# Kernel tuning notes

Hardware: AMD Instinct MI355X
Metric: run time of the kernel (lower is better)

The kernel has to match this reference:

```python
import jax, jax.numpy as jnp
import numpy as np
from jax import lax

B, N, K, NUM_CLASS = 8, 4096, 16, 13


def knn(pc, k):
    # pc: (B, C, N); returns indices of k nearest neighbors (B, N, k)
    sq = jnp.sum(pc * pc, axis=1)                       # (B, N)
    inner = jnp.einsum('bcn,bcm->bnm', pc, pc)          # (B, N, N)
    neg_dist = 2.0 * inner - sq[:, :, None] - sq[:, None, :]
    return lax.top_k(neg_dist, k)[1]                    # (B, N, k)


def group(fea, idx):
    # fea: (B, C, N), idx: (B, N, k) -> (B, C, N, k)
    return jax.vmap(lambda f, i: f[:, i])(fea, idx)


def mlp2(x, w, b, act=True):
    # 1x1 conv2d: x (B, Cin, N, k) -> (B, Cout, N, k)
    y = jnp.einsum('oc,bcnk->bonk', w, x) + b[None, :, None, None]
    return jax.nn.relu(y) if act else y


def mlp1(x, w, b, act=True):
    # 1x1 conv1d: x (B, Cin, N) -> (B, Cout, N)
    y = jnp.einsum('oc,bcn->bon', w, x) + b[None, :, None]
    return jax.nn.relu(y) if act else y


def edgeconv(xyz, fea, k, wg1, bg1, wg2, bg2, wf1, bf1, wf2, bf2, wf3, bf3):
    idx = knn(fea, k)
    # geometric branch: (B, 10, N, k) = [dist, xyz, xyz_knn, xyz - xyz_knn]
    xk = group(xyz, idx)
    xc = jnp.broadcast_to(xyz[:, :, :, None], xk.shape)
    xr = xc - xk
    xd = jnp.sqrt(jnp.sum(xr * xr, axis=1, keepdims=True))
    g = jnp.concatenate([xd, xc, xk, xr], axis=1)
    # feature branch: (B, 2C, N, k) = [fea, fea_knn]
    fk = group(fea, idx)
    fc = jnp.broadcast_to(fea[:, :, :, None], fk.shape)
    f = jnp.concatenate([fc, fk], axis=1)
    g = mlp2(mlp2(g, wg1, bg1), wg2, bg2)
    f = mlp2(mlp2(mlp2(f, wf1, bf1), wf2, bf2), wf3, bf3)
    return jnp.max(g * f, axis=-1)  # (B, Cout, N)


_SPECS = [
    ('e1_mg1', 10, 32), ('e1_mg2', 32, 32),
    ('e1_mf1', 6, 32), ('e1_mf2', 32, 32), ('e1_mf3', 32, 32),
    ('e2_mg1', 10, 128), ('e2_mg2', 128, 128),
    ('e2_mf1', 64, 128), ('e2_mf2', 128, 128), ('e2_mf3', 128, 128),
    ('c1', 128, 128), ('c2', 128, 1024), ('c3', 1184, 512),
    ('c4', 512, 256), ('c5', 256, 128), ('c6', 128, NUM_CLASS),
]


def setup_inputs() -> dict:
    key = jax.random.key(0)
    ks = jax.random.split(key, 2 * len(_SPECS) + 1)
    inp = {'xyz': jax.random.normal(ks[0], (B, N, 3), dtype=jnp.float32)}
    for j, (name, ci, co) in enumerate(_SPECS):
        scale = 1.0 / np.sqrt(ci)
        inp['w_' + name] = jax.random.normal(ks[2 * j + 1], (co, ci), dtype=jnp.float32) * scale
        inp['b_' + name] = jax.random.normal(ks[2 * j + 2], (co,), dtype=jnp.float32) * 0.01
    return inp


def reference(xyz, w_e1_mg1, b_e1_mg1, w_e1_mg2, b_e1_mg2, w_e1_mf1, b_e1_mf1,
              w_e1_mf2, b_e1_mf2, w_e1_mf3, b_e1_mf3, w_e2_mg1, b_e2_mg1,
              w_e2_mg2, b_e2_mg2, w_e2_mf1, b_e2_mf1, w_e2_mf2, b_e2_mf2,
              w_e2_mf3, b_e2_mf3, w_c1, b_c1, w_c2, b_c2, w_c3, b_c3,
              w_c4, b_c4, w_c5, b_c5, w_c6, b_c6):
    x = jnp.transpose(xyz, (0, 2, 1))  # (B, 3, N)
    fea1 = edgeconv(x, x, K, w_e1_mg1, b_e1_mg1, w_e1_mg2, b_e1_mg2,
                    w_e1_mf1, b_e1_mf1, w_e1_mf2, b_e1_mf2, w_e1_mf3, b_e1_mf3)
    fea2 = edgeconv(x, fea1, K, w_e2_mg1, b_e2_mg1, w_e2_mg2, b_e2_mg2,
                    w_e2_mf1, b_e2_mf1, w_e2_mf2, b_e2_mf2, w_e2_mf3, b_e2_mf3)
    f = mlp1(fea2, w_c1, b_c1)
    f = mlp1(f, w_c2, b_c2)                        # (B, 1024, N)
    g = jnp.max(f, axis=-1, keepdims=True)         # global feature (B, 1024, 1)
    g = jnp.broadcast_to(g, (g.shape[0], g.shape[1], x.shape[2]))
    f = jnp.concatenate([fea1, fea2, g], axis=1)   # (B, 1184, N)
    f = mlp1(f, w_c3, b_c3)
    f = mlp1(f, w_c4, b_c4)
    f = mlp1(f, w_c5, b_c5)
    return mlp1(f, w_c6, b_c6, act=False)          # (B, NUM_CLASS, N)
```

## Files before the change

kernel.cpp:

```cpp
#include <hip/hip_runtime.h>
#include <math.h>

#define B_ 8
#define N_ 4096
#define PL_ (8 * 4096 * 32)

__device__ __forceinline__ unsigned short bf16rne(float x) {
    unsigned int u = __float_as_uint(x);
    return (unsigned short)((u + 0x7FFFu + ((u >> 16) & 1u)) >> 16);
}
__device__ __forceinline__ float bff(unsigned short h) {
    return __uint_as_float((unsigned int)h << 16);
}
__device__ __forceinline__ void cvt_hl(unsigned short* base, int numel, int idx, float x) {
    unsigned short h = bf16rne(x);
    base[idx] = h;
    base[numel + idx] = bf16rne(x - bff(h));
}

typedef __attribute__((ext_vector_type(8))) short bf16x8;
typedef __attribute__((ext_vector_type(4))) float f32x4;

#define MF16(a, b, c) __builtin_amdgcn_mfma_f32_16x16x32_bf16((a), (b), (c), 0, 0, 0)

__global__ __launch_bounds__(256) void prep_kernel(
    const float* __restrict__ w0, const float* __restrict__ w1,
    const float* __restrict__ w2, const float* __restrict__ w3,
    const float* __restrict__ w4, const float* __restrict__ w5,
    const float* __restrict__ w6, const float* __restrict__ w8,
    const float* __restrict__ w9, const float* __restrict__ w10,
    const float* __restrict__ w11, const float* __restrict__ w12,
    const float* __restrict__ w13, const float* __restrict__ w14,
    const float* __restrict__ wf1, const float* __restrict__ bf1,
    const float* __restrict__ xyz,
    float* __restrict__ wt, float* __restrict__ gbuf, float* __restrict__ sqbuf,
    unsigned short* __restrict__ xyzp) {
    const int g = blockIdx.x * 256 + threadIdx.x;
    unsigned short* wus = (unsigned short*)(wt + 3840);

    if (g < 3584) {
        if (g < 320)       { int i = g >> 5, o = g & 31;             wt[g] = w0[o * 10 + i]; }
        else if (g < 1344) { int l = g - 320;  int i = l >> 5, o = l & 31; wt[g] = w1[o * 32 + i]; }
        else if (g < 1536) { int l = g - 1344; int i = l >> 5, o = l & 31; wt[g] = w2[o * 6 + i]; }
        else if (g < 2560) { int l = g - 1536; int i = l >> 5, o = l & 31; wt[g] = w3[o * 32 + i]; }
        else               { int l = g - 2560; int i = l >> 5, o = l & 31; wt[g] = w4[o * 32 + i]; }
    }
    else if (g < 3840)   { int l = g - 3584; wt[g] = (l < 128) ? bf1[l] : 0.0f; }
    else if (g < 12032)  { int l = g - 3840; int o = l >> 5, i = l & 31;
                           float x = (o < 128) ? wf1[o * 64 + i] : wf1[(o - 128) * 64 + 32 + i];
                           cvt_hl(wus + 0, 8192, l, x); }
    else if (g < 28416)  { int l = g - 12032;  cvt_hl(wus + 16384, 16384, l, w10[l]); }
    else if (g < 159488) { int l = g - 28416;  cvt_hl(wus + 49152, 131072, l, w11[l]); }
    else if (g < 241408) { int l = g - 159488; int o = l / 160, i = l - o * 160;
                           cvt_hl(wus + 311296, 81920, l, w12[o * 1184 + i]); }
    else if (g < 372480) { int l = g - 241408; cvt_hl(wus + 475136, 131072, l, w13[l]); }
    else if (g < 405248) { int l = g - 372480; cvt_hl(wus + 737280, 32768, l, w14[l]); }
    else if (g < 409344) { int l = g - 405248; int o = l >> 5, k = l & 31;
                           float x = (k < 10) ? w5[o * 10 + k] : 0.0f;
                           cvt_hl(wus + 802816, 4096, l, x); }
    else if (g < 425728) { int l = g - 409344; cvt_hl(wus + 811008, 16384, l, w6[l]); }
    else if (g < 442112) { int l = g - 425728; cvt_hl(wus + 843776, 16384, l, w8[l]); }
    else if (g < 458496) { int l = g - 442112; cvt_hl(wus + 876544, 16384, l, w9[l]); }
    else if (g < 466688) { gbuf[g - 458496] = 0.0f; }
    else if (g < 499456) { int l = g - 466688;
                           const float* p = xyz + (size_t)l * 3;
                           sqbuf[l] = fmaf(p[0], p[0], fmaf(p[1], p[1], p[2] * p[2])); }
    else if (g < 532224) {
        int row = g - 499456;
        const float* p = xyz + (size_t)row * 3;
        unsigned short hv[8] = {0,0,0,0,0,0,0,0};
        unsigned short mv[8] = {0,0,0,0,0,0,0,0};
        unsigned short lv[8] = {0,0,0,0,0,0,0,0};
        #pragma unroll
        for (int c = 0; c < 3; ++c) {
            float v = p[c];
            unsigned short h = bf16rne(v); float d = v - bff(h);
            unsigned short m = bf16rne(d);
            hv[c] = h; mv[c] = m; lv[c] = bf16rne(d - bff(m));
        }
        uint4 z = make_uint4(0u, 0u, 0u, 0u);
        unsigned short* d0 = xyzp + (size_t)row * 32;
        unsigned short* d1 = d0 + PL_;
        unsigned short* d2 = d0 + 2 * PL_;
        *(uint4*)d0 = *(uint4*)hv; *(uint4*)(d0 + 8) = z; *(uint4*)(d0 + 16) = z; *(uint4*)(d0 + 24) = z;
        *(uint4*)d1 = *(uint4*)mv; *(uint4*)(d1 + 8) = z; *(uint4*)(d1 + 16) = z; *(uint4*)(d1 + 24) = z;
        *(uint4*)d2 = *(uint4*)lv; *(uint4*)(d2 + 8) = z; *(uint4*)(d2 + 16) = z; *(uint4*)(d2 + 24) = z;
    }
}

__global__ __launch_bounds__(256) void fea1p_kernel(
    const float* __restrict__ F, unsigned short* __restrict__ P, float* __restrict__ SQ) {
    int row = blockIdx.x * 256 + threadIdx.x;
    const float* x = F + (size_t)row * 32;
    float s = 0.0f;
    unsigned short hb[32], mb[32], lb[32];
    #pragma unroll
    for (int c = 0; c < 32; ++c) {
        float v = x[c];
        s = fmaf(v, v, s);
        unsigned short h = bf16rne(v); float d = v - bff(h);
        unsigned short m = bf16rne(d);
        hb[c] = h; mb[c] = m; lb[c] = bf16rne(d - bff(m));
    }
    SQ[row] = s;
    unsigned short* d0 = P + (size_t)row * 32;
    #pragma unroll
    for (int q = 0; q < 4; ++q) {
        *(uint4*)(d0 + 8 * q)           = *(uint4*)&hb[8 * q];
        *(uint4*)(d0 + PL_ + 8 * q)     = *(uint4*)&mb[8 * q];
        *(uint4*)(d0 + 2 * PL_ + 8 * q) = *(uint4*)&lb[8 * q];
    }
}


__device__ __forceinline__ void cas_asc(unsigned long long& x, unsigned long long& y) {
    unsigned long long a = x, b = y;
    bool sw = a > b;
    x = sw ? b : a;
    y = sw ? a : b;
}

__device__ __forceinline__ void merge_top(unsigned long long (&k)[16],
                                          const unsigned long long (&o)[16]) {
    #pragma unroll
    for (int i = 0; i < 16; ++i) {
        unsigned long long bb = o[15 - i];
        if (bb > k[i]) k[i] = bb;
    }
    #pragma unroll
    for (int st = 8; st >= 1; st >>= 1)
        #pragma unroll
        for (int i = 0; i < 16; ++i)
            if ((i & st) == 0) cas_asc(k[i], k[i + st]);
}

__device__ __forceinline__ void merge_idx_row(
    const unsigned long long* __restrict__ Kbuf, int b, int row, int* __restrict__ dst) {
    unsigned long long K0[16], K1[16];
    const unsigned long long* p0 = Kbuf + (((size_t)b * 2 + 0) * N_ + row) * 16;
    const unsigned long long* p1 = Kbuf + (((size_t)b * 2 + 1) * N_ + row) * 16;
    #pragma unroll
    for (int j = 0; j < 16; ++j) { K0[j] = p0[j]; K1[j] = p1[j]; }
    merge_top(K0, K1);
    #pragma unroll
    for (int j = 0; j < 16; ++j)
        dst[j] = 4095 - (int)(unsigned int)(K0[15 - j] & 0xFFFFFFFFu);
}

__device__ __forceinline__ void casv(float& x, float& y) {
    float lo = fminf(x, y), hi = fmaxf(x, y);
    x = lo; y = hi;
}

__device__ __forceinline__ void sortv16(float (&v)[16]) {
    #pragma unroll
    for (int sz = 2; sz <= 16; sz <<= 1)
        #pragma unroll
        for (int st = sz >> 1; st >= 1; st >>= 1)
            #pragma unroll
            for (int i = 0; i < 16; ++i)
                if ((i & st) == 0) {
                    if ((i & sz) == 0) casv(v[i], v[i + st]);
                    else                casv(v[i + st], v[i]);
                }
}

__device__ __forceinline__ void mergev(float (&kv)[16], const float (&nv)[16]) {
    #pragma unroll
    for (int i = 0; i < 16; ++i) kv[i] = fmaxf(kv[i], nv[15 - i]);
    #pragma unroll
    for (int st = 8; st >= 1; st >>= 1)
        #pragma unroll
        for (int i = 0; i < 16; ++i)
            if ((i & st) == 0) casv(kv[i], kv[i + st]);
}

__global__ __launch_bounds__(512, 2) void knn_kernel(
    const unsigned short* __restrict__ P, const float* __restrict__ SQ,
    unsigned long long* __restrict__ Kout) {
    __shared__ __align__(16) unsigned short Bs[3][64][40];
    __shared__ __align__(16) char U[34816];
    __shared__ float tau_sm[128];
    __shared__ int cnt[128];
    const int t = threadIdx.x;
    const int b = blockIdx.y;
    const int r0 = blockIdx.x * 128;
    const int half = blockIdx.z;
    const int H0 = half * 2048;
    const int lane = t & 63, w = t >> 6;
    const int lr = lane & 15, lg = lane >> 4;
    const int kb = lg << 3;
    const int sc = t >> 3, sq2 = (t & 7) << 2;

    float* Ds = (float*)U + w * 1088;
    unsigned long long* cap = (unsigned long long*)U;

    const unsigned short* ap = P + ((size_t)(b * N_) + r0 + 16 * w + lr) * 32 + kb;
    const bf16x8 ah = *(const bf16x8*)ap;
    const bf16x8 am = *(const bf16x8*)(ap + PL_);
    const bf16x8 al = *(const bf16x8*)(ap + 2 * PL_);
    const f32x4 sqr4 = *(const f32x4*)&SQ[(size_t)b * N_ + r0 + 16 * w + 4 * lg];

    const float* SQc = SQ + (size_t)b * N_ + H0;
    const unsigned short* Pc = P + ((size_t)(b * N_) + H0) * 32;

    uint2 sgh, sgm, sgl;
    auto issue = [&](int tt) {
        const unsigned short* src = Pc + (size_t)(tt * 64 + sc) * 32 + sq2;
        sgh = *(const uint2*)src;
        sgm = *(const uint2*)(src + PL_);
        sgl = *(const uint2*)(src + 2 * PL_);
    };
    auto commit = [&]() {
        *(uint2*)&Bs[0][sc][sq2] = sgh;
        *(uint2*)&Bs[1][sc][sq2] = sgm;
        *(uint2*)&Bs[2][sc][sq2] = sgl;
    };

    float kv[16];
    #pragma unroll
    for (int j = 0; j < 16; ++j) kv[j] = -3.4e38f;

    issue(0);
    for (int tt = 0; tt < 32; ++tt) {
        commit();
        __syncthreads();
        if (tt + 1 < 32) issue(tt + 1);
        #pragma unroll
        for (int j = 0; j < 4; ++j) {
            int cc = 16 * j + lr;
            bf16x8 bh = *(const bf16x8*)&Bs[0][cc][kb];
            bf16x8 bm = *(const bf16x8*)&Bs[1][cc][kb];
            bf16x8 bl = *(const bf16x8*)&Bs[2][cc][kb];
            f32x4 a = {0.0f, 0.0f, 0.0f, 0.0f};
            a = MF16(ah, bh, a); a = MF16(am, bh, a); a = MF16(ah, bm, a);
            a = MF16(am, bm, a); a = MF16(al, bh, a); a = MF16(ah, bl, a);
            float sqcv = SQc[tt * 64 + cc];
            #pragma unroll
            for (int r = 0; r < 4; ++r)
                Ds[(4 * lg + r) * 68 + cc] = fmaf(2.0f, a[r], -sqr4[r]) - sqcv;
        }
        float nv[16];
        #pragma unroll
        for (int q = 0; q < 4; ++q)
            *(float4*)&nv[4 * q] = *(const float4*)&Ds[lr * 68 + lg * 16 + 4 * q];
        sortv16(nv);
        mergev(kv, nv);
        __syncthreads();
    }
    issue(0);

    #pragma unroll
    for (int st = 16; st <= 32; st <<= 1) {
        float ov[16];
        #pragma unroll
        for (int i = 0; i < 16; ++i) ov[i] = __shfl_xor(kv[15 - i], st);
        #pragma unroll
        for (int i = 0; i < 16; ++i) kv[i] = fmaxf(kv[i], ov[i]);
        #pragma unroll
        for (int s2 = 8; s2 >= 1; s2 >>= 1)
            #pragma unroll
            for (int i = 0; i < 16; ++i)
                if ((i & s2) == 0) casv(kv[i], kv[i + s2]);
    }
    if (lane < 16) { tau_sm[w * 16 + lane] = kv[0]; cnt[w * 16 + lane] = 0; }
    const f32x4 taur4 = *(const f32x4*)&tau_sm[w * 16 + 4 * lg];

    for (int tt = 0; tt < 32; ++tt) {
        commit();
        __syncthreads();
        if (tt + 1 < 32) issue(tt + 1);
        #pragma unroll
        for (int j = 0; j < 4; ++j) {
            int cc = 16 * j + lr;
            bf16x8 bh = *(const bf16x8*)&Bs[0][cc][kb];
            bf16x8 bm = *(const bf16x8*)&Bs[1][cc][kb];
            bf16x8 bl = *(const bf16x8*)&Bs[2][cc][kb];
            f32x4 a = {0.0f, 0.0f, 0.0f, 0.0f};
            a = MF16(ah, bh, a); a = MF16(am, bh, a); a = MF16(ah, bm, a);
            a = MF16(am, bm, a); a = MF16(al, bh, a); a = MF16(ah, bl, a);
            float sqcv = SQc[tt * 64 + cc];
            #pragma unroll
            for (int r = 0; r < 4; ++r) {
                float e = fmaf(2.0f, a[r], -sqr4[r]) - sqcv;
                if (e >= taur4[r]) {
                    int row = 16 * w + 4 * lg + r;
                    unsigned int u = __float_as_uint(e);
                    unsigned int ou = (u & 0x80000000u) ? ~u : (u | 0x80000000u);
                    unsigned long long key = ((unsigned long long)ou << 32)
                                           | (unsigned int)(4095 - (H0 + tt * 64 + cc));
                    int pos = atomicAdd(&cnt[row], 1);
                    if (pos < 32) cap[row * 32 + pos] = key;
                }
            }
        }
        __syncthreads();
    }

    if (t < 128) {
        int n = min(cnt[t], 32);
        unsigned long long K[16];
        #pragma unroll
        for (int j = 0; j < 16; ++j) K[j] = 0ull;
        for (int i = 0; i < n; ++i) {
            unsigned long long v = cap[t * 32 + i];
            if (v > K[0]) {
                K[0] = v;
                #pragma unroll
                for (int s = 0; s < 15; ++s) cas_asc(K[s], K[s + 1]);
            }
        }
        size_t obase = (((size_t)b * 2 + half) * N_ + r0 + t) * 16;
        #pragma unroll
        for (int j = 0; j < 16; ++j) Kout[obase + j] = K[j];
    }
}


__global__ __launch_bounds__(256, 4) void e1_kernel(
    const float* __restrict__ xyz, const unsigned long long* __restrict__ Kbuf,
    const float* __restrict__ wte1,
    const float* __restrict__ bg1, const float* __restrict__ bg2,
    const float* __restrict__ bf1, const float* __restrict__ bf2,
    const float* __restrict__ bf3,
    float* __restrict__ fea1) {
    __shared__ __align__(16) float Ain[10 * 132];
    __shared__ __align__(16) float Bu0[32 * 132];
    __shared__ __align__(16) float Bu1[32 * 132];
    __shared__ __align__(16) float wl[3584];
    __shared__ float bl[5][32];
    __shared__ __align__(16) float Pm1[4][8][32];
    __shared__ int idxl[128];
    const int t = threadIdx.x;
    const int b = blockIdx.x >> 9;
    const int n0 = (blockIdx.x & 511) << 3;
    const int et = (t & 31) << 2;
    const int ct = (t >> 5) << 2;

    for (int i = t; i < 3584; i += 256) wl[i] = wte1[i];
    if (t < 32) {
        bl[0][t] = bg1[t]; bl[1][t] = bg2[t]; bl[2][t] = bf1[t];
        bl[3][t] = bf2[t]; bl[4][t] = bf3[t];
    }
    if (t < 8) merge_idx_row(Kbuf, b, n0 + t, &idxl[t * 16]);
    __syncthreads();
    if (t < 128) {
        int p = t >> 4, n = n0 + p, m = idxl[t];
        const float* xc = xyz + ((size_t)b * N_ + n) * 3;
        const float* xk = xyz + ((size_t)b * N_ + m) * 3;
        float c0 = xc[0], c1v = xc[1], c2v = xc[2];
        float k0 = xk[0], k1 = xk[1], k2 = xk[2];
        float r0 = c0 - k0, r1 = c1v - k1, r2 = c2v - k2;
        Ain[0 * 132 + t] = sqrtf(r0 * r0 + r1 * r1 + r2 * r2);
        Ain[1 * 132 + t] = c0;  Ain[2 * 132 + t] = c1v; Ain[3 * 132 + t] = c2v;
        Ain[4 * 132 + t] = k0;  Ain[5 * 132 + t] = k1;  Ain[6 * 132 + t] = k2;
        Ain[7 * 132 + t] = r0;  Ain[8 * 132 + t] = r1;  Ain[9 * 132 + t] = r2;
    }
    __syncthreads();

    float acc[4][4];
    auto gem = [&](int KK, const float* Asrc, int woff) {
        #pragma unroll
        for (int ii = 0; ii < 4; ++ii)
            #pragma unroll
            for (int jj = 0; jj < 4; ++jj) acc[ii][jj] = 0.0f;
        for (int i = 0; i < KK; ++i) {
            float a4[4], w4[4];
            *(float4*)a4 = *(const float4*)&Asrc[i * 132 + et];
            *(float4*)w4 = *(const float4*)&wl[woff + i * 32 + ct];
            #pragma unroll
            for (int ii = 0; ii < 4; ++ii)
                #pragma unroll
                for (int jj = 0; jj < 4; ++jj)
                    acc[ii][jj] = fmaf(a4[ii], w4[jj], acc[ii][jj]);
        }
    };
    auto wrout = [&](float* dst, const float* brow) {
        #pragma unroll
        for (int jj = 0; jj < 4; ++jj) {
            float tmp[4];
            #pragma unroll
            for (int ii = 0; ii < 4; ++ii) tmp[ii] = fmaxf(acc[ii][jj] + brow[ct + jj], 0.0f);
            *(float4*)&dst[(ct + jj) * 132 + et] = *(float4*)tmp;
        }
    };

    gem(10, Ain, 0);          wrout(Bu1, bl[0]);   __syncthreads();
    gem(32, Bu1, 320);
    float g2r[4][4];
    #pragma unroll
    for (int ii = 0; ii < 4; ++ii)
        #pragma unroll
        for (int jj = 0; jj < 4; ++jj)
            g2r[ii][jj] = fmaxf(acc[ii][jj] + bl[1][ct + jj], 0.0f);
    gem(6, Ain + 132, 1344);  wrout(Bu0, bl[2]);   __syncthreads();
    gem(32, Bu0, 1536);       wrout(Bu1, bl[3]);   __syncthreads();
    gem(32, Bu1, 2560);

    float pm[4];
    #pragma unroll
    for (int jj = 0; jj < 4; ++jj) {
        float mx = 0.0f;
        #pragma unroll
        for (int ii = 0; ii < 4; ++ii) {
            float f3 = fmaxf(acc[ii][jj] + bl[4][ct + jj], 0.0f);
            mx = fmaxf(mx, g2r[ii][jj] * f3);
        }
        pm[jj] = mx;
    }
    const int sub = t & 3, pl = (t & 31) >> 2;
    *(float4*)&Pm1[sub][pl][ct] = *(float4*)pm;
    __syncthreads();
    {
        int p = t >> 5, c = t & 31;
        float v = fmaxf(fmaxf(Pm1[0][p][c], Pm1[1][p][c]), fmaxf(Pm1[2][p][c], Pm1[3][p][c]));
        fea1[((size_t)b * N_ + n0 + p) * 32 + c] = v;
    }
}


__global__ __launch_bounds__(256, 2) void e2_kernel(
    const float* __restrict__ xyz, const unsigned long long* __restrict__ Kbuf,
    const float* __restrict__ CfPf,
    const unsigned short* __restrict__ wg1p, const unsigned short* __restrict__ wg2p,
    const unsigned short* __restrict__ wf2p, const unsigned short* __restrict__ wf3p,
    const float* __restrict__ bg1, const float* __restrict__ bg2,
    const float* __restrict__ bf2, const float* __restrict__ bf3,
    float* __restrict__ fea2) {
    __shared__ __align__(16) unsigned short Ah[128 * 128];
    __shared__ __align__(16) unsigned short Al[128 * 128];
    __shared__ float bb[4][128];
    __shared__ int idxl[128];
    const int t = threadIdx.x;
    const int b = blockIdx.x >> 9;
    const int n0 = (blockIdx.x & 511) << 3;
    const int lane = t & 63, w = t >> 6;
    const int wr = w << 5;
    const int lr = lane & 15, lg = lane >> 4;
    const int kb = lg << 3;

    auto swz = [](int e, int bo) { return e * 256 + (bo ^ ((e & 7) << 4)); };

    for (int i = t; i < 512; i += 256) {
        const float* bp = (i < 128) ? bg1 : (i < 256) ? bg2 : (i < 384) ? bf2 : bf3;
        bb[i >> 7][i & 127] = bp[i & 127];
    }
    if (t < 8) merge_idx_row(Kbuf, b, n0 + t, &idxl[t * 16]);
    __syncthreads();

    f32x4 acc[2][8];
    const f32x4 zz = {0.0f, 0.0f, 0.0f, 0.0f};
    auto zacc = [&]() {
        #pragma unroll
        for (int i = 0; i < 2; ++i)
            #pragma unroll
            for (int j = 0; j < 8; ++j) acc[i][j] = zz;
    };

    {
        zacc();
        bf16x8 wh[2], wl_[2];
        #pragma unroll
        for (int i = 0; i < 2; ++i) {
            size_t off = (size_t)(wr + i * 16 + lr) * 32 + kb;
            wh[i] = *(const bf16x8*)(wg1p + off);
            wl_[i] = *(const bf16x8*)(wg1p + 4096 + off);
        }
        #pragma unroll
        for (int j = 0; j < 8; ++j) {
            float gv[8];
            #pragma unroll
            for (int q = 0; q < 8; ++q) gv[q] = 0.0f;
            if (lg < 2) {
                int e = j * 16 + lr;
                int p = e >> 4, m = idxl[e];
                const float* xc = xyz + ((size_t)b * N_ + n0 + p) * 3;
                const float* xk = xyz + ((size_t)b * N_ + m) * 3;
                float c0 = xc[0], c1 = xc[1], c2 = xc[2];
                float k0 = xk[0], k1 = xk[1], k2 = xk[2];
                float r0 = c0 - k0, r1 = c1 - k1, r2 = c2 - k2;
                if (lg == 0) {
                    gv[0] = sqrtf(r0 * r0 + r1 * r1 + r2 * r2);
                    gv[1] = c0; gv[2] = c1; gv[3] = c2;
                    gv[4] = k0; gv[5] = k1; gv[6] = k2; gv[7] = r0;
                } else { gv[0] = r1; gv[1] = r2; }
            }
            bf16x8 gbh, gbl;
            #pragma unroll
            for (int q = 0; q < 8; ++q) {
                unsigned short h = bf16rne(gv[q]);
                gbh[q] = (short)h;
                gbl[q] = (short)bf16rne(gv[q] - bff(h));
            }
            #pragma unroll
            for (int i = 0; i < 2; ++i) {
                acc[i][j] = MF16(wh[i], gbh, acc[i][j]);
                acc[i][j] = MF16(wl_[i], gbh, acc[i][j]);
                acc[i][j] = MF16(wh[i], gbl, acc[i][j]);
            }
        }
    }

    auto epi_store = [&](const float* brow) {
        #pragma unroll
        for (int i = 0; i < 2; ++i) {
            int o4 = wr + i * 16 + lg * 4;
            float bv[4];
            *(float4*)bv = *(const float4*)&brow[o4];
            #pragma unroll
            for (int j = 0; j < 8; ++j) {
                int e = j * 16 + lr;
                unsigned short h[4], l[4];
                #pragma unroll
                for (int r = 0; r < 4; ++r) {
                    float v = fmaxf(acc[i][j][r] + bv[r], 0.0f);
                    h[r] = bf16rne(v);
                    l[r] = bf16rne(v - bff(h[r]));
                }
                int bo = swz(e, o4 * 2);
                *(ushort4*)((char*)Ah + bo) = make_ushort4(h[0], h[1], h[2], h[3]);
                *(ushort4*)((char*)Al + bo) = make_ushort4(l[0], l[1], l[2], l[3]);
            }
        }
    };
    epi_store(bb[0]);
    __syncthreads();

    auto gemmK = [&](const unsigned short* __restrict__ Wp) {
        zacc();
        #pragma unroll
        for (int ks = 0; ks < 4; ++ks) {
            bf16x8 wh[2], wl_[2];
            #pragma unroll
            for (int i = 0; i < 2; ++i) {
                size_t off = (size_t)(wr + i * 16 + lr) * 128 + ks * 32 + kb;
                wh[i] = *(const bf16x8*)(Wp + off);
                wl_[i] = *(const bf16x8*)(Wp + 16384 + off);
            }
            #pragma unroll
            for (int jh = 0; jh < 2; ++jh) {
                bf16x8 xh[4], xl[4];
                #pragma unroll
                for (int jj = 0; jj < 4; ++jj) {
                    int e = (jh * 4 + jj) * 16 + lr;
                    int bo = swz(e, (ks * 32 + kb) * 2);
                    xh[jj] = *(const bf16x8*)((const char*)Ah + bo);
                    xl[jj] = *(const bf16x8*)((const char*)Al + bo);
                }
                #pragma unroll
                for (int i = 0; i < 2; ++i) {
                    #pragma unroll
                    for (int jj = 0; jj < 4; ++jj) {
                        int j = jh * 4 + jj;
                        acc[i][j] = MF16(wh[i], xh[jj], acc[i][j]);
                        acc[i][j] = MF16(wl_[i], xh[jj], acc[i][j]);
                        acc[i][j] = MF16(wh[i], xl[jj], acc[i][j]);
                    }
                }
            }
        }
    };

    gemmK(wg2p);
    float g2r[2][8][4];
    #pragma unroll
    for (int i = 0; i < 2; ++i) {
        float bv[4];
        *(float4*)bv = *(const float4*)&bb[1][wr + i * 16 + lg * 4];
        #pragma unroll
        for (int j = 0; j < 8; ++j)
            #pragma unroll
            for (int r = 0; r < 4; ++r)
                g2r[i][j][r] = fmaxf(acc[i][j][r] + bv[r], 0.0f);
    }
    __syncthreads();

    {
        int e = t & 127, hf = t >> 7;
        int n = n0 + (e >> 4), m = idxl[e];
        const float* crow = CfPf + ((size_t)b * N_ + n) * 256 + hf * 64;
        const float* prow = CfPf + ((size_t)b * N_ + m) * 256 + 128 + hf * 64;
        #pragma unroll
        for (int q = 0; q < 16; ++q) {
            float4 cc = *(const float4*)(crow + q * 4);
            float4 pp = *(const float4*)(prow + q * 4);
            float v[4] = { fmaxf(cc.x + pp.x, 0.0f), fmaxf(cc.y + pp.y, 0.0f),
                           fmaxf(cc.z + pp.z, 0.0f), fmaxf(cc.w + pp.w, 0.0f) };
            unsigned short h[4], l[4];
            #pragma unroll
            for (int r = 0; r < 4; ++r) {
                h[r] = bf16rne(v[r]);
                l[r] = bf16rne(v[r] - bff(h[r]));
            }
            int bo = swz(e, (hf * 64 + q * 4) * 2);
            *(ushort4*)((char*)Ah + bo) = make_ushort4(h[0], h[1], h[2], h[3]);
            *(ushort4*)((char*)Al + bo) = make_ushort4(l[0], l[1], l[2], l[3]);
        }
    }
    __syncthreads();

    gemmK(wf2p);
    __syncthreads();
    epi_store(bb[2]);
    __syncthreads();

    gemmK(wf3p);
    #pragma unroll
    for (int j = 0; j < 8; ++j) {
        int p = j;
        #pragma unroll
        for (int i = 0; i < 2; ++i) {
            int o4 = wr + i * 16 + lg * 4;
            float bv[4];
            *(float4*)bv = *(const float4*)&bb[3][o4];
            float vr[4];
            #pragma unroll
            for (int r = 0; r < 4; ++r) {
                float f3v = fmaxf(acc[i][j][r] + bv[r], 0.0f);
                float v = g2r[i][j][r] * f3v;
                v = fmaxf(v, __shfl_xor(v, 1));
                v = fmaxf(v, __shfl_xor(v, 2));
                v = fmaxf(v, __shfl_xor(v, 4));
                v = fmaxf(v, __shfl_xor(v, 8));
                vr[r] = v;
            }
            if (lr == 0)
                *(float4*)(fea2 + ((size_t)b * N_ + n0 + p) * 128 + o4) = *(float4*)vr;
        }
    }
}


template<int RELU, int BMODE, int GMAX>
__global__ __launch_bounds__(256) void gemm_mfma(
    const float* __restrict__ X1, int S1, int K1,
    const float* __restrict__ X2, int S2, int Ktot,
    const unsigned short* __restrict__ Wc, const float* __restrict__ bias,
    float* __restrict__ Y, int COUT, float* __restrict__ gout) {
    __shared__ __align__(16) unsigned short Xh[128 * 40];
    __shared__ __align__(16) unsigned short Xl[128 * 40];
    __shared__ __align__(16) unsigned short Wh[128 * 40];
    __shared__ __align__(16) unsigned short Wl[128 * 40];
    __shared__ float Gm[2][128];
    const int t = threadIdx.x;
    const int m0 = blockIdx.x * 128, o0 = blockIdx.y * 128;
    const int lane = t & 63, w = t >> 6;
    const int wr = (w >> 1) << 6, wc = (w & 1) << 6;
    const int lr = lane & 15, lg = lane >> 4;
    const int kb = lg << 3;
    const size_t WN = (size_t)COUT * Ktot;

    f32x4 acc[4][4];
    const f32x4 zz = {0.0f, 0.0f, 0.0f, 0.0f};
    #pragma unroll
    for (int i = 0; i < 4; ++i)
        #pragma unroll
        for (int j = 0; j < 4; ++j) acc[i][j] = zz;

    const int ntile = Ktot >> 5;
    for (int kt = 0; kt < ntile; ++kt) {
        const int kbase = kt << 5;
        const float* Xp; int S, koff;
        if (kbase < K1) { Xp = X1; S = S1; koff = kbase; }
        else            { Xp = X2; S = S2; koff = kbase - K1; }
        #pragma unroll
        for (int rr = 0; rr < 4; ++rr) {
            int idx = t + rr * 256;
            int p = idx >> 3, i4 = (idx & 7) << 2;
            const float4 v = *(const float4*)(Xp + (size_t)(m0 + p) * S + koff + i4);
            unsigned short h0 = bf16rne(v.x), h1 = bf16rne(v.y);
            unsigned short h2 = bf16rne(v.z), h3 = bf16rne(v.w);
            *(ushort4*)&Xh[p * 40 + i4] = make_ushort4(h0, h1, h2, h3);
            *(ushort4*)&Xl[p * 40 + i4] = make_ushort4(
                bf16rne(v.x - bff(h0)), bf16rne(v.y - bff(h1)),
                bf16rne(v.z - bff(h2)), bf16rne(v.w - bff(h3)));
        }
        #pragma unroll
        for (int rr = 0; rr < 2; ++rr) {
            int c = t + rr * 256;
            int o = c >> 2, k8 = (c & 3) << 3;
            const unsigned short* src = Wc + (size_t)(o0 + o) * Ktot + kbase + k8;
            *(uint4*)&Wh[o * 40 + k8] = *(const uint4*)src;
            *(uint4*)&Wl[o * 40 + k8] = *(const uint4*)(src + WN);
        }
        __syncthreads();

        bf16x8 ah[4], al[4], bh[4], bl[4];
        #pragma unroll
        for (int f = 0; f < 4; ++f) {
            ah[f] = *(const bf16x8*)&Xh[(wr + f * 16 + lr) * 40 + kb];
            al[f] = *(const bf16x8*)&Xl[(wr + f * 16 + lr) * 40 + kb];
            bh[f] = *(const bf16x8*)&Wh[(wc + f * 16 + lr) * 40 + kb];
            bl[f] = *(const bf16x8*)&Wl[(wc + f * 16 + lr) * 40 + kb];
        }
        #pragma unroll
        for (int i = 0; i < 4; ++i)
            #pragma unroll
            for (int j = 0; j < 4; ++j) {
                acc[i][j] = MF16(ah[i], bh[j], acc[i][j]);
                acc[i][j] = MF16(al[i], bh[j], acc[i][j]);
                acc[i][j] = MF16(ah[i], bl[j], acc[i][j]);
            }
        __syncthreads();
    }

    const int b = m0 >> 12;
    if (GMAX) {
        #pragma unroll
        for (int j = 0; j < 4; ++j) {
            const int oc = wc + j * 16 + lr;
            const float bv = bias[o0 + oc];
            float mx = 0.0f;
            #pragma unroll
            for (int i = 0; i < 4; ++i)
                #pragma unroll
                for (int r = 0; r < 4; ++r) {
                    float v = acc[i][j][r] + bv;
                    if (RELU) v = fmaxf(v, 0.0f);
                    mx = fmaxf(mx, v);
                }
            mx = fmaxf(mx, __shfl_xor(mx, 16));
            mx = fmaxf(mx, __shfl_xor(mx, 32));
            if (lane < 16) Gm[w >> 1][wc + j * 16 + lane] = mx;
        }
        __syncthreads();
        if (t < 128) {
            float v = fmaxf(Gm[0][t], Gm[1][t]);
            atomicMax((unsigned int*)(gout + b * 1024 + o0 + t), __float_as_uint(v));
        }
    } else {
        #pragma unroll
        for (int j = 0; j < 4; ++j) {
            const int oc = wc + j * 16 + lr;
            const float bv = (BMODE == 0) ? bias[o0 + oc] : bias[b * 512 + o0 + oc];
            #pragma unroll
            for (int i = 0; i < 4; ++i) {
                float* yp = Y + (size_t)(m0 + wr + i * 16 + lg * 4) * COUT + o0 + oc;
                #pragma unroll
                for (int r = 0; r < 4; ++r) {
                    float v = acc[i][j][r] + bv;
                    if (RELU) v = fmaxf(v, 0.0f);
                    yp[(size_t)r * COUT] = v;
                }
            }
        }
    }
}


__global__ void bias3_kernel(const float* __restrict__ g, const float* __restrict__ w_c3,
                             const float* __restrict__ b_c3, float* __restrict__ bias3) {
    __shared__ float gs[1024];
    int b = blockIdx.x >> 1;
    int o = ((blockIdx.x & 1) << 8) + threadIdx.x;
    for (int i = threadIdx.x; i < 1024; i += 256) gs[i] = g[b * 1024 + i];
    __syncthreads();
    float acc = b_c3[o];
    const float* wr = w_c3 + (size_t)o * 1184 + 160;
    for (int i = 0; i < 1024; i += 4) {
        float4 w4 = *(const float4*)(wr + i);
        acc = fmaf(w4.x, gs[i], acc);     acc = fmaf(w4.y, gs[i + 1], acc);
        acc = fmaf(w4.z, gs[i + 2], acc); acc = fmaf(w4.w, gs[i + 3], acc);
    }
    bias3[b * 512 + o] = acc;
}


__global__ __launch_bounds__(256, 1) void c6_kernel(
    const float* __restrict__ h5, const float* __restrict__ w,
    const float* __restrict__ bias, float* __restrict__ out) {
    __shared__ float ws[13 * 128];
    __shared__ float bs[13];
    int t = threadIdx.x;
    for (int i = t; i < 13 * 128; i += 256) ws[i] = w[i];
    if (t < 13) bs[t] = bias[t];
    __syncthreads();
    int b = blockIdx.x >> 4;
    int n = ((blockIdx.x & 15) << 8) + t;
    float x[128];
    const float* xp = h5 + ((size_t)b * N_ + n) * 128;
    #pragma unroll
    for (int i = 0; i < 128; i += 4) *(float4*)&x[i] = *(const float4*)(xp + i);
    for (int o = 0; o < 13; ++o) {
        float acc = bs[o];
        #pragma unroll
        for (int i = 0; i < 128; ++i) acc = fmaf(ws[o * 128 + i], x[i], acc);
        out[((size_t)b * 13 + o) * N_ + n] = acc;
    }
}


extern "C" void kernel_launch(void* const* d_in, const int* in_sizes, int n_in,
                              void* d_out, int out_size, void* d_ws, size_t ws_size,
                              hipStream_t stream) {
    (void)in_sizes; (void)n_in; (void)out_size; (void)ws_size;
    const float* xyz = (const float*)d_in[0];
    #define W_(j)  ((const float*)d_in[1 + 2 * (j)])
    #define Bp_(j) ((const float*)d_in[2 + 2 * (j)])

    char* ws = (char*)d_ws;
    const size_t MB = 1u << 20;
    float* fea1  = (float*)(ws + 4 * MB);
    float* CfPf  = (float*)(ws + 8 * MB);
    float* fea2  = (float*)(ws + 40 * MB);
    float* h1    = (float*)(ws + 56 * MB);
    float* sqbuf = (float*)(ws + 72 * MB);
    float* gbuf  = (float*)(ws + 72 * MB + (128u << 10));
    float* b3buf = (float*)(ws + 72 * MB + (160u << 10));
    float* wt    = (float*)(ws + 72 * MB + (176u << 10));
    float* h3    = (float*)(ws + 75 * MB);
    float* h4    = CfPf;
    float* h5    = h1;
    float* outp  = (float*)d_out;
    unsigned long long* Kbuf = (unsigned long long*)(ws + 75 * MB);
    unsigned short* xyzp = (unsigned short*)(ws + 8 * MB);
    unsigned short* feap = (unsigned short*)(ws + 14 * MB);

    float* wte1  = wt;
    float* bpre  = wt + 3584;
    const unsigned short* wus = (const unsigned short*)(wt + 3840);
    const unsigned short* wpre = wus + 0;
    const unsigned short* wc1  = wus + 16384;
    const unsigned short* wc2  = wus + 49152;
    const unsigned short* wc3  = wus + 311296;
    const unsigned short* wc4  = wus + 475136;
    const unsigned short* wc5  = wus + 737280;
    const unsigned short* wg1p = wus + 802816;
    const unsigned short* wg2p = wus + 811008;
    const unsigned short* wf2p = wus + 843776;
    const unsigned short* wf3p = wus + 876544;

    prep_kernel<<<2079, 256, 0, stream>>>(
        W_(0), W_(1), W_(2), W_(3), W_(4), W_(5), W_(6), W_(8), W_(9), W_(10),
        W_(11), W_(12), W_(13), W_(14), W_(7), Bp_(7), xyz, wt, gbuf, sqbuf, xyzp);

    knn_kernel<<<dim3(32, 8, 2), 512, 0, stream>>>(xyzp, sqbuf, Kbuf);
    e1_kernel<<<4096, 256, 0, stream>>>(xyz, Kbuf, wte1, Bp_(0), Bp_(1), Bp_(2), Bp_(3), Bp_(4), fea1);

    fea1p_kernel<<<128, 256, 0, stream>>>(fea1, feap, sqbuf);
    knn_kernel<<<dim3(32, 8, 2), 512, 0, stream>>>(feap, sqbuf, Kbuf);
    gemm_mfma<0, 0, 0><<<dim3(256, 2), 256, 0, stream>>>(fea1, 32, 32, nullptr, 0, 32,
                                                         wpre, bpre, CfPf, 256, nullptr);
    e2_kernel<<<4096, 256, 0, stream>>>(xyz, Kbuf, CfPf, wg1p, wg2p, wf2p, wf3p,
                                        Bp_(5), Bp_(6), Bp_(8), Bp_(9), fea2);

    gemm_mfma<1, 0, 0><<<dim3(256, 1), 256, 0, stream>>>(fea2, 128, 128, nullptr, 0, 128,
                                                         wc1, Bp_(10), h1, 128, nullptr);
    gemm_mfma<1, 0, 1><<<dim3(256, 8), 256, 0, stream>>>(h1, 128, 128, nullptr, 0, 128,
                                                         wc2, Bp_(11), nullptr, 1024, gbuf);
    bias3_kernel<<<16, 256, 0, stream>>>(gbuf, W_(12), Bp_(12), b3buf);
    gemm_mfma<1, 1, 0><<<dim3(256, 4), 256, 0, stream>>>(fea1, 32, 32, fea2, 128, 160,
                                                         wc3, b3buf, h3, 512, nullptr);
    gemm_mfma<1, 0, 0><<<dim3(256, 2), 256, 0, stream>>>(h3, 512, 512, nullptr, 0, 512,
                                                         wc4, Bp_(13), h4, 256, nullptr);
    gemm_mfma<1, 0, 0><<<dim3(256, 1), 256, 0, stream>>>(h4, 256, 256, nullptr, 0, 256,
                                                         wc5, Bp_(14), h5, 128, nullptr);
    c6_kernel<<<128, 256, 0, stream>>>(h5, W_(15), Bp_(15), outp);
    #undef W_
    #undef Bp_
}
```

Baseline: 1.049 ms.

## Split e2_kernel across 8 waves, each owning 16 output channels

Doubles the e2_kernel block from 256 to 512 threads. Each wave now computes 16 output channels instead of 32, which halves the per-thread accumulator and g2r register arrays. The staging loops for biases and the gathered feature rows are redistributed across the extra threads. The aim is more waves per CU and less register pressure, at the cost of each wave reading the shared-memory activation tile for fewer output rows, which means more LDS traffic per MFMA.

New measurement: 1.055 ms. No clear change (+0.6%).

```diff
diff --git a/kernel.cpp b/kernel.cpp
--- a/kernel.cpp
+++ b/kernel.cpp
@@ -419,7 +419,7 @@
 }
 
 
-__global__ __launch_bounds__(256, 2) void e2_kernel(
+__global__ __launch_bounds__(512, 2) void e2_kernel(
     const float* __restrict__ xyz, const unsigned long long* __restrict__ Kbuf,
     const float* __restrict__ CfPf,
     const unsigned short* __restrict__ wg1p, const unsigned short* __restrict__ wg2p,
@@ -435,36 +435,33 @@
     const int b = blockIdx.x >> 9;
     const int n0 = (blockIdx.x & 511) << 3;
     const int lane = t & 63, w = t >> 6;
-    const int wr = w << 5;
+    const int wr = w << 4;
     const int lr = lane & 15, lg = lane >> 4;
     const int kb = lg << 3;
 
     auto swz = [](int e, int bo) { return e * 256 + (bo ^ ((e & 7) << 4)); };
 
-    for (int i = t; i < 512; i += 256) {
-        const float* bp = (i < 128) ? bg1 : (i < 256) ? bg2 : (i < 384) ? bf2 : bf3;
-        bb[i >> 7][i & 127] = bp[i & 127];
+    {
+        const float* bp = (t < 128) ? bg1 : (t < 256) ? bg2 : (t < 384) ? bf2 : bf3;
+        bb[t >> 7][t & 127] = bp[t & 127];
     }
     if (t < 8) merge_idx_row(Kbuf, b, n0 + t, &idxl[t * 16]);
     __syncthreads();
 
-    f32x4 acc[2][8];
+    f32x4 acc[8];
     const f32x4 zz = {0.0f, 0.0f, 0.0f, 0.0f};
     auto zacc = [&]() {
         #pragma unroll
-        for (int i = 0; i < 2; ++i)
-            #pragma unroll
-            for (int j = 0; j < 8; ++j) acc[i][j] = zz;
+        for (int j = 0; j < 8; ++j) acc[j] = zz;
     };
 
     {
         zacc();
-        bf16x8 wh[2], wl_[2];
-        #pragma unroll
-        for (int i = 0; i < 2; ++i) {
-            size_t off = (size_t)(wr + i * 16 + lr) * 32 + kb;
-            wh[i] = *(const bf16x8*)(wg1p + off);
-            wl_[i] = *(const bf16x8*)(wg1p + 4096 + off);
+        bf16x8 wh, wl_;
+        {
+            size_t off = (size_t)(wr + lr) * 32 + kb;
+            wh = *(const bf16x8*)(wg1p + off);
+            wl_ = *(const bf16x8*)(wg1p + 4096 + off);
         }
         #pragma unroll
         for (int j = 0; j < 8; ++j) {
@@ -492,35 +489,29 @@
                 gbh[q] = (short)h;
                 gbl[q] = (short)bf16rne(gv[q] - bff(h));
             }
-            #pragma unroll
-            for (int i = 0; i < 2; ++i) {
-                acc[i][j] = MF16(wh[i], gbh, acc[i][j]);
-                acc[i][j] = MF16(wl_[i], gbh, acc[i][j]);
-                acc[i][j] = MF16(wh[i], gbl, acc[i][j]);
-            }
+            acc[j] = MF16(wh, gbh, acc[j]);
+            acc[j] = MF16(wl_, gbh, acc[j]);
+            acc[j] = MF16(wh, gbl, acc[j]);
         }
     }
 
     auto epi_store = [&](const float* brow) {
-        #pragma unroll
-        for (int i = 0; i < 2; ++i) {
-            int o4 = wr + i * 16 + lg * 4;
-            float bv[4];
-            *(float4*)bv = *(const float4*)&brow[o4];
-            #pragma unroll
-            for (int j = 0; j < 8; ++j) {
-                int e = j * 16 + lr;
-                unsigned short h[4], l[4];
-                #pragma unroll
-                for (int r = 0; r < 4; ++r) {
-                    float v = fmaxf(acc[i][j][r] + bv[r], 0.0f);
-                    h[r] = bf16rne(v);
-                    l[r] = bf16rne(v - bff(h[r]));
-                }
-                int bo = swz(e, o4 * 2);
-                *(ushort4*)((char*)Ah + bo) = make_ushort4(h[0], h[1], h[2], h[3]);
-                *(ushort4*)((char*)Al + bo) = make_ushort4(l[0], l[1], l[2], l[3]);
-            }
+        int o4 = wr + lg * 4;
+        float bv[4];
+        *(float4*)bv = *(const float4*)&brow[o4];
+        #pragma unroll
+        for (int j = 0; j < 8; ++j) {
+            int e = j * 16 + lr;
+            unsigned short h[4], l[4];
+            #pragma unroll
+            for (int r = 0; r < 4; ++r) {
+                float v = fmaxf(acc[j][r] + bv[r], 0.0f);
+                h[r] = bf16rne(v);
+                l[r] = bf16rne(v - bff(h[r]));
+            }
+            int bo = swz(e, o4 * 2);
+            *(ushort4*)((char*)Ah + bo) = make_ushort4(h[0], h[1], h[2], h[3]);
+            *(ushort4*)((char*)Al + bo) = make_ushort4(l[0], l[1], l[2], l[3]);
         }
     };
     epi_store(bb[0]);
@@ -530,12 +521,11 @@
         zacc();
         #pragma unroll
         for (int ks = 0; ks < 4; ++ks) {
-            bf16x8 wh[2], wl_[2];
-            #pragma unroll
-            for (int i = 0; i < 2; ++i) {
-                size_t off = (size_t)(wr + i * 16 + lr) * 128 + ks * 32 + kb;
-                wh[i] = *(const bf16x8*)(Wp + off);
-                wl_[i] = *(const bf16x8*)(Wp + 16384 + off);
+            bf16x8 wh, wl_;
+            {
+                size_t off = (size_t)(wr + lr) * 128 + ks * 32 + kb;
+                wh = *(const bf16x8*)(Wp + off);
+                wl_ = *(const bf16x8*)(Wp + 16384 + off);
             }
             #pragma unroll
             for (int jh = 0; jh < 2; ++jh) {
@@ -548,40 +538,36 @@
                     xl[jj] = *(const bf16x8*)((const char*)Al + bo);
                 }
                 #pragma unroll
-                for (int i = 0; i < 2; ++i) {
-                    #pragma unroll
-                    for (int jj = 0; jj < 4; ++jj) {
-                        int j = jh * 4 + jj;
-                        acc[i][j] = MF16(wh[i], xh[jj], acc[i][j]);
-                        acc[i][j] = MF16(wl_[i], xh[jj], acc[i][j]);
-                        acc[i][j] = MF16(wh[i], xl[jj], acc[i][j]);
-                    }
+                for (int jj = 0; jj < 4; ++jj) {
+                    int j = jh * 4 + jj;
+                    acc[j] = MF16(wh, xh[jj], acc[j]);
+                    acc[j] = MF16(wl_, xh[jj], acc[j]);
+                    acc[j] = MF16(wh, xl[jj], acc[j]);
                 }
             }
         }
     };
 
     gemmK(wg2p);
-    float g2r[2][8][4];
-    #pragma unroll
-    for (int i = 0; i < 2; ++i) {
+    float g2r[8][4];
+    {
         float bv[4];
-        *(float4*)bv = *(const float4*)&bb[1][wr + i * 16 + lg * 4];
+        *(float4*)bv = *(const float4*)&bb[1][wr + lg * 4];
         #pragma unroll
         for (int j = 0; j < 8; ++j)
             #pragma unroll
             for (int r = 0; r < 4; ++r)
-                g2r[i][j][r] = fmaxf(acc[i][j][r] + bv[r], 0.0f);
+                g2r[j][r] = fmaxf(acc[j][r] + bv[r], 0.0f);
     }
     __syncthreads();
 
     {
         int e = t & 127, hf = t >> 7;
         int n = n0 + (e >> 4), m = idxl[e];
-        const float* crow = CfPf + ((size_t)b * N_ + n) * 256 + hf * 64;
-        const float* prow = CfPf + ((size_t)b * N_ + m) * 256 + 128 + hf * 64;
-        #pragma unroll
-        for (int q = 0; q < 16; ++q) {
+        const float* crow = CfPf + ((size_t)b * N_ + n) * 256 + hf * 32;
+        const float* prow = CfPf + ((size_t)b * N_ + m) * 256 + 128 + hf * 32;
+        #pragma unroll
+        for (int q = 0; q < 8; ++q) {
             float4 cc = *(const float4*)(crow + q * 4);
             float4 pp = *(const float4*)(prow + q * 4);
             float v[4] = { fmaxf(cc.x + pp.x, 0.0f), fmaxf(cc.y + pp.y, 0.0f),
@@ -592,7 +578,7 @@
                 h[r] = bf16rne(v[r]);
                 l[r] = bf16rne(v[r] - bff(h[r]));
             }
-            int bo = swz(e, (hf * 64 + q * 4) * 2);
+            int bo = swz(e, (hf * 32 + q * 4) * 2);
             *(ushort4*)((char*)Ah + bo) = make_ushort4(h[0], h[1], h[2], h[3]);
             *(ushort4*)((char*)Al + bo) = make_ushort4(l[0], l[1], l[2], l[3]);
         }
@@ -605,19 +591,17 @@
     __syncthreads();
 
     gemmK(wf3p);
-    #pragma unroll
-    for (int j = 0; j < 8; ++j) {
-        int p = j;
-        #pragma unroll
-        for (int i = 0; i < 2; ++i) {
-            int o4 = wr + i * 16 + lg * 4;
-            float bv[4];
-            *(float4*)bv = *(const float4*)&bb[3][o4];
+    {
+        int o4 = wr + lg * 4;
+        float bv[4];
+        *(float4*)bv = *(const float4*)&bb[3][o4];
+        #pragma unroll
+        for (int j = 0; j < 8; ++j) {
             float vr[4];
             #pragma unroll
             for (int r = 0; r < 4; ++r) {
-                float f3v = fmaxf(acc[i][j][r] + bv[r], 0.0f);
-                float v = g2r[i][j][r] * f3v;
+                float f3v = fmaxf(acc[j][r] + bv[r], 0.0f);
+                float v = g2r[j][r] * f3v;
                 v = fmaxf(v, __shfl_xor(v, 1));
                 v = fmaxf(v, __shfl_xor(v, 2));
                 v = fmaxf(v, __shfl_xor(v, 4));
@@ -625,7 +609,7 @@
                 vr[r] = v;
             }
             if (lr == 0)
-                *(float4*)(fea2 + ((size_t)b * N_ + n0 + p) * 128 + o4) = *(float4*)vr;
+                *(float4*)(fea2 + ((size_t)b * N_ + n0 + j) * 128 + o4) = *(float4*)vr;
         }
     }
 }
@@ -841,7 +825,7 @@
     knn_kernel<<<dim3(32, 8, 2), 512, 0, stream>>>(feap, sqbuf, Kbuf);
     gemm_mfma<0, 0, 0><<<dim3(256, 2), 256, 0, stream>>>(fea1, 32, 32, nullptr, 0, 32,
                                                          wpre, bpre, CfPf, 256, nullptr);
-    e2_kernel<<<4096, 256, 0, stream>>>(xyz, Kbuf, CfPf, wg1p, wg2p, wf2p, wf3p,
+    e2_kernel<<<4096, 512, 0, stream>>>(xyz, Kbuf, CfPf, wg1p, wg2p, wf2p, wf3p,
                                         Bp_(5), Bp_(6), Bp_(8), Bp_(9), fea2);
 
     gemm_mfma<1, 0, 0><<<dim3(256, 1), 256, 0, stream>>>(fea2, 128, 128, nullptr, 0, 128,
```
